# Performance work log

Hardware: AMD Instinct MI355X
Metric: run time of the kernel (lower is better)

Reference implementation:

```python
import jax, jax.numpy as jnp
import numpy as np

DIM = 1024
HEADS = 16
HEAD_DIM = 64
INNER = HEADS * HEAD_DIM  # 1024
SCALE = 8.0
LN_EPS = 1e-5
NORM_EPS = 1e-12  # F.normalize default eps


def layer_norm(x, g, b):
    m = jnp.mean(x, axis=-1, keepdims=True)
    v = jnp.mean((x - m) ** 2, axis=-1, keepdims=True)
    return (x - m) * jax.lax.rsqrt(v + LN_EPS) * g + b


def l2_normalize(x):
    n = jnp.sqrt(jnp.sum(x * x, axis=-1, keepdims=True))
    return x / jnp.maximum(n, NORM_EPS)


def setup_inputs() -> dict:
    key = jax.random.key(0)
    ks = jax.random.split(key, 8)
    B, N, T = 4, 4096, 256
    s = 0.02
    return {
        "x": jax.random.normal(ks[0], (B, N, DIM), jnp.float32),
        "context": jax.random.normal(ks[1], (B, T, DIM), jnp.float32),
        "Wq": jax.random.normal(ks[2], (DIM, INNER), jnp.float32) * s,
        "Wkv": jax.random.normal(ks[3], (DIM, 2 * INNER), jnp.float32) * s,
        "Wo": jax.random.normal(ks[4], (INNER, DIM), jnp.float32) * s,
        "null_kv": jax.random.normal(ks[5], (2, HEAD_DIM), jnp.float32),
        "q_scale": jnp.ones((HEAD_DIM,), jnp.float32),
        "k_scale": jnp.ones((HEAD_DIM,), jnp.float32),
        "ln_in_g": jnp.ones((DIM,), jnp.float32),
        "ln_in_b": jnp.zeros((DIM,), jnp.float32),
        "ln_ctx_g": jnp.ones((DIM,), jnp.float32),
        "ln_ctx_b": jnp.zeros((DIM,), jnp.float32),
        "ln_out_g": jnp.ones((DIM,), jnp.float32),
        "ln_out_b": jnp.zeros((DIM,), jnp.float32),
    }


def reference(x, context, Wq, Wkv, Wo, null_kv, q_scale, k_scale,
              ln_in_g, ln_in_b, ln_ctx_g, ln_ctx_b, ln_out_g, ln_out_b):
    B, N, _ = x.shape
    T = context.shape[1]
    xn = layer_norm(x, ln_in_g, ln_in_b)
    cn = layer_norm(context, ln_ctx_g, ln_ctx_b)
    q = xn @ Wq                      # [B, N, INNER]
    kv = cn @ Wkv                    # [B, T, 2*INNER]
    k, v = jnp.split(kv, 2, axis=-1)
    # split heads: b s (h d) -> b h s d
    def split_heads(t):
        b, s, _ = t.shape
        return t.reshape(b, s, HEADS, HEAD_DIM).transpose(0, 2, 1, 3)
    q, k, v = split_heads(q), split_heads(k), split_heads(v)
    # null kv token appended along kv-seq dim
    nk = jnp.broadcast_to(null_kv[0], (B, HEADS, 1, HEAD_DIM))
    nv = jnp.broadcast_to(null_kv[1], (B, HEADS, 1, HEAD_DIM))
    k = jnp.concatenate([k, nk], axis=2)   # [B, H, T+1, D]
    v = jnp.concatenate([v, nv], axis=2)
    q = l2_normalize(q) * q_scale
    k = l2_normalize(k) * k_scale
    scores = jnp.einsum('bhid,bhkd->bhik', q, k) * SCALE
    attn = jax.nn.softmax(scores, axis=-1)
    out = jnp.einsum('bhik,bhkd->bhid', attn, v)   # [B, H, N, D]
    out = out.transpose(0, 2, 1, 3).reshape(B, N, INNER)
    out = out @ Wo
    return layer_norm(out, ln_out_g, ln_out_b)
```

## Files before the change

### kernel.cpp

```cpp
#include <hip/hip_runtime.h>
#include <cstdint>
#include <cstddef>

typedef _Float16 f16;
typedef _Float16 f16x4 __attribute__((ext_vector_type(4)));
typedef _Float16 f16x8 __attribute__((ext_vector_type(8)));
typedef float f32x4 __attribute__((ext_vector_type(4)));
typedef __fp16 h16x2 __attribute__((ext_vector_type(2)));

#define DIM 1024
#define B_ 4
#define N_ 4096
#define TKP 288
#define SCALE_ 8.0f
#define LOG2E 1.4426950408889634f

__device__ __forceinline__ void gload_lds16(const void* g, void* l) {
  __builtin_amdgcn_global_load_lds(
      reinterpret_cast<const __attribute__((address_space(1))) uint32_t*>(
          reinterpret_cast<uintptr_t>(g)),
      reinterpret_cast<__attribute__((address_space(3))) uint32_t*>(
          reinterpret_cast<uintptr_t>(l)),
      16, 0, 0);
}

__global__ void transpose_w_kernel(const float* __restrict__ W, f16* __restrict__ WT,
                                   int K, int N) {
  __shared__ float tile[32][33];
  int nt = N >> 5;
  int tk = blockIdx.x / nt, tn = blockIdx.x % nt;
  int tx = threadIdx.x & 31, ty = threadIdx.x >> 5;
#pragma unroll
  for (int p = 0; p < 32; p += 8)
    tile[ty + p][tx] = W[(size_t)(tk * 32 + ty + p) * N + tn * 32 + tx];
  __syncthreads();
#pragma unroll
  for (int p = 0; p < 32; p += 8)
    WT[(size_t)(tn * 32 + ty + p) * K + tk * 32 + tx] = (f16)tile[tx][ty + p];
}

template <typename IN_T, typename OUT_T>
__global__ void ln_kernel(const IN_T* __restrict__ in, const float* __restrict__ g,
                          const float* __restrict__ bb, OUT_T* __restrict__ out) {
  int row = blockIdx.x;
  int t = threadIdx.x;
  float4 v;
  if constexpr (sizeof(IN_T) == 2) {
    f16x4 h = ((const f16x4*)((const f16*)in + (size_t)row * DIM))[t];
    v = {(float)h[0], (float)h[1], (float)h[2], (float)h[3]};
  } else {
    v = ((const float4*)((const float*)in + (size_t)row * DIM))[t];
  }
  float s = v.x + v.y + v.z + v.w;
  float ss = v.x * v.x + v.y * v.y + v.z * v.z + v.w * v.w;
#pragma unroll
  for (int m = 1; m < 64; m <<= 1) { s += __shfl_xor(s, m); ss += __shfl_xor(ss, m); }
  __shared__ float red[8];
  int w = t >> 6;
  if ((t & 63) == 0) { red[w * 2] = s; red[w * 2 + 1] = ss; }
  __syncthreads();
  s = red[0] + red[2] + red[4] + red[6];
  ss = red[1] + red[3] + red[5] + red[7];
  float mean = s * (1.0f / DIM);
  float var = ss * (1.0f / DIM) - mean * mean;
  float rstd = rsqrtf(var + 1e-5f);
  float4 gv = ((const float4*)g)[t];
  float4 bv = ((const float4*)bb)[t];
  float o0 = (v.x - mean) * rstd * gv.x + bv.x;
  float o1 = (v.y - mean) * rstd * gv.y + bv.y;
  float o2 = (v.z - mean) * rstd * gv.z + bv.z;
  float o3 = (v.w - mean) * rstd * gv.w + bv.w;
  if constexpr (sizeof(OUT_T) == 2) {
    f16x4 h = {(f16)o0, (f16)o1, (f16)o2, (f16)o3};
    *(f16x4*)((f16*)out + (size_t)row * DIM + t * 4) = h;
  } else {
    float4 o = {o0, o1, o2, o3};
    *(float4*)((float*)out + (size_t)row * DIM + t * 4) = o;
  }
}

template <bool OUT_F32>
__global__ __launch_bounds__(256, 2) void gemm_nt_kernel(
    const f16* __restrict__ A, const f16* __restrict__ Bt, void* __restrict__ C,
    int M, int N, int K) {
  __shared__ f16 As[128 * 64];
  __shared__ f16 Bs[128 * 64];
  int nb = N >> 7;
  int cpx = gridDim.x >> 3;
  int wg = ((int)blockIdx.x & 7) * cpx + ((int)blockIdx.x >> 3);
  int bm = wg / nb, bn = wg % nb;
  int t = threadIdx.x;
  int lane = t & 63, w = t >> 6;
  int wm = w >> 1, wn = w & 1;
  int r16 = lane & 15, g4 = lane >> 4;
  f32x4 acc[4][4] = {};
  for (int k0 = 0; k0 < K; k0 += 64) {
#pragma unroll
    for (int i = 0; i < 4; ++i) {
      int li = i * 256 + t;
      int r = li >> 3, c = li & 7;
      int kc = ((c ^ (r & 7)) << 3);
      gload_lds16(A + (size_t)(bm * 128 + r) * K + k0 + kc, (char*)As + li * 16);
      gload_lds16(Bt + (size_t)(bn * 128 + r) * K + k0 + kc, (char*)Bs + li * 16);
    }
    asm volatile("s_waitcnt vmcnt(0)" ::: "memory");
    __syncthreads();
#pragma unroll
    for (int ks = 0; ks < 2; ++ks) {
      f16x8 af[4], bf[4];
#pragma unroll
      for (int mi = 0; mi < 4; ++mi) {
        int r = wm * 64 + mi * 16 + r16;
        int cidx = ks * 4 + g4;
        af[mi] = *(const f16x8*)(As + r * 64 + ((cidx ^ (r & 7)) << 3));
      }
#pragma unroll
      for (int ni = 0; ni < 4; ++ni) {
        int r = wn * 64 + ni * 16 + r16;
        int cidx = ks * 4 + g4;
        bf[ni] = *(const f16x8*)(Bs + r * 64 + ((cidx ^ (r & 7)) << 3));
      }
#pragma unroll
      for (int mi = 0; mi < 4; ++mi)
#pragma unroll
        for (int ni = 0; ni < 4; ++ni)
          acc[mi][ni] = __builtin_amdgcn_mfma_f32_16x16x32_f16(af[mi], bf[ni],
                                                               acc[mi][ni], 0, 0, 0);
    }
    __syncthreads();
  }
  int cr0 = bm * 128 + wm * 64;
  int cc = bn * 128 + wn * 64 + r16;
#pragma unroll
  for (int mi = 0; mi < 4; ++mi)
#pragma unroll
    for (int ni = 0; ni < 4; ++ni)
#pragma unroll
      for (int j = 0; j < 4; ++j) {
        int row = cr0 + mi * 16 + g4 * 4 + j;
        int col = cc + ni * 16;
        if constexpr (OUT_F32)
          ((float*)C)[(size_t)row * N + col] = acc[mi][ni][j];
        else
          ((f16*)C)[(size_t)row * N + col] = (f16)acc[mi][ni][j];
      }
}

__global__ void prep_kv_kernel(const f16* __restrict__ kv, const float* __restrict__ nullkv,
                               const float* __restrict__ ks, f16* __restrict__ Karr,
                               f16* __restrict__ Varr) {
  int bh = blockIdx.x;
  int b = bh >> 4, h = bh & 15;
  int t = threadIdx.x;
  __shared__ f16 vt[256][65];
  const f16* krow = kv + (size_t)(b * 256 + t) * 2048 + h * 64;
  const f16* vrow = krow + 1024;
  f16x8 kd[8];
  float ss = 0.0f;
#pragma unroll
  for (int i = 0; i < 8; ++i) {
    kd[i] = *(const f16x8*)(krow + i * 8);
#pragma unroll
    for (int j = 0; j < 8; ++j) { float x = (float)kd[i][j]; ss += x * x; }
  }
  float inv = 1.0f / fmaxf(sqrtf(ss), 1e-12f);
  f16* kout = Karr + ((size_t)bh * TKP + t) * 64;
#pragma unroll
  for (int i = 0; i < 8; ++i) {
    f16x8 o;
#pragma unroll
    for (int j = 0; j < 8; ++j) o[j] = (f16)((float)kd[i][j] * inv * ks[i * 8 + j]);
    *(f16x8*)(kout + i * 8) = o;
  }
#pragma unroll
  for (int i = 0; i < 8; ++i) {
    f16x8 vv = *(const f16x8*)(vrow + i * 8);
#pragma unroll
    for (int j = 0; j < 8; ++j) vt[t][i * 8 + j] = vv[j];
  }
  if (t < 32) {
    f16* kr = Karr + ((size_t)bh * TKP + 256 + t) * 64;
    if (t == 0) {
      float ssn = 0.0f;
      for (int d = 0; d < 64; ++d) ssn += nullkv[d] * nullkv[d];
      float invn = 1.0f / fmaxf(sqrtf(ssn), 1e-12f);
      for (int d = 0; d < 64; ++d) kr[d] = (f16)(nullkv[d] * invn * ks[d]);
    } else {
      for (int d = 0; d < 64; ++d) kr[d] = (f16)0.0f;
    }
  }
  __syncthreads();
  f16* vbase = Varr + (size_t)bh * 64 * TKP;
  int pcol = (t & ~31) | (((t & 15) << 1) | ((t >> 4) & 1));
  for (int d = 0; d < 64; ++d) vbase[(size_t)d * TKP + pcol] = vt[t][d];
#pragma unroll
  for (int i = 0; i < 8; ++i) {
    int idx = i * 256 + t;
    int d = idx >> 5, key = 256 + (idx & 31);
    vbase[(size_t)d * TKP + key] = (key == 256) ? (f16)nullkv[64 + d] : (f16)0.0f;
  }
}

__global__ __launch_bounds__(256, 4) void attn_kernel(
    const f16* __restrict__ Q, const f16* __restrict__ Karr,
    const f16* __restrict__ Varr, const float* __restrict__ qs,
    const float* __restrict__ ksc, f16* __restrict__ O) {
  int wgid = ((int)blockIdx.x & 7) * 256 + ((int)blockIdx.x >> 3);
  int qb = wgid & 31, bh = wgid >> 5;
  int b = bh >> 4, h = bh & 15;
  int t = threadIdx.x, lane = t & 63, w = t >> 6;
  int r16 = lane & 15, g4 = lane >> 4;
  int row0 = b * N_ + qb * 128 + w * 32;
  int col0 = h * 64;
  const f16* Kp = Karr + (size_t)bh * TKP * 64;
  const f16* Vp = Varr + (size_t)bh * 64 * TKP;
  __shared__ f16 Plds[4][32 * 40];
  f16* Pw = &Plds[w][0];
  float mq = fabsf(qs[lane]), mk = fabsf(ksc[lane]);
#pragma unroll
  for (int m = 1; m < 64; m <<= 1) {
    mq = fmaxf(mq, __shfl_xor(mq, m));
    mk = fmaxf(mk, __shfl_xor(mk, m));
  }
  const float c1 = SCALE_ * LOG2E;
  const float c2 = SCALE_ * mq * mk * LOG2E;
  float qsv[2][8];
#pragma unroll
  for (int kdh = 0; kdh < 2; ++kdh)
#pragma unroll
    for (int i = 0; i < 8; ++i) qsv[kdh][i] = qs[kdh * 32 + g4 * 8 + i];
  f16x8 qf[2][2];
#pragma unroll
  for (int mi = 0; mi < 2; ++mi) {
    float f[2][8];
    float ssq = 0.0f;
#pragma unroll
    for (int kdh = 0; kdh < 2; ++kdh) {
      f16x8 v = *(const f16x8*)(Q + (size_t)(row0 + mi * 16 + r16) * DIM +
                                col0 + kdh * 32 + g4 * 8);
#pragma unroll
      for (int i = 0; i < 8; ++i) { f[kdh][i] = (float)v[i]; ssq += f[kdh][i] * f[kdh][i]; }
    }
    ssq += __shfl_xor(ssq, 16);
    ssq += __shfl_xor(ssq, 32);
    float inv = 1.0f / fmaxf(sqrtf(ssq), 1e-12f);
#pragma unroll
    for (int kdh = 0; kdh < 2; ++kdh) {
      f16x8 o;
#pragma unroll
      for (int i = 0; i < 8; ++i) o[i] = (f16)(f[kdh][i] * inv * qsv[kdh][i]);
      qf[mi][kdh] = o;
    }
  }
  f32x4 o[2][4] = {};
  float part[2][4] = {};
  const h16x2 ones2 = {(__fp16)1.0f, (__fp16)1.0f};
  f16x8 kf[2][2];
#pragma unroll
  for (int ni = 0; ni < 2; ++ni)
#pragma unroll
    for (int kdh = 0; kdh < 2; ++kdh)
      kf[ni][kdh] = *(const f16x8*)(Kp + (size_t)(ni * 16 + r16) * 64 +
                                    kdh * 32 + g4 * 8);
  for (int kt = 0; kt < 9; ++kt) {
    int key0 = kt * 32;
    f16x8 vf[4];
#pragma unroll
    for (int nd = 0; nd < 4; ++nd)
      vf[nd] = *(const f16x8*)(Vp + (size_t)(nd * 16 + r16) * TKP + key0 + g4 * 8);
    float nb0 = (key0 + r16 <= 256) ? -c2 : -(c2 + 128.0f);
    float nb1 = (key0 + 16 + r16 <= 256) ? -c2 : -(c2 + 128.0f);
    f32x4 s[2][2] = {};
    __builtin_amdgcn_s_setprio(1);
#pragma unroll
    for (int kdh = 0; kdh < 2; ++kdh)
#pragma unroll
      for (int mi = 0; mi < 2; ++mi)
#pragma unroll
        for (int ni = 0; ni < 2; ++ni)
          s[mi][ni] = __builtin_amdgcn_mfma_f32_16x16x32_f16(qf[mi][kdh], kf[ni][kdh],
                                                             s[mi][ni], 0, 0, 0);
    __builtin_amdgcn_s_setprio(0);
    if (kt < 8) {
#pragma unroll
      for (int ni = 0; ni < 2; ++ni)
#pragma unroll
        for (int kdh = 0; kdh < 2; ++kdh)
          kf[ni][kdh] = *(const f16x8*)(Kp + (size_t)(key0 + 32 + ni * 16 + r16) * 64 +
                                        kdh * 32 + g4 * 8);
    }
#pragma unroll
    for (int mi = 0; mi < 2; ++mi) {
#pragma unroll
      for (int j = 0; j < 4; ++j) {
        float p0 = __builtin_amdgcn_exp2f(s[mi][0][j] * c1 + nb0);
        float p1 = __builtin_amdgcn_exp2f(s[mi][1][j] * c1 + nb1);
        h16x2 pk = __builtin_amdgcn_cvt_pkrtz(p0, p1);
        part[mi][j] = __builtin_amdgcn_fdot2(pk, ones2, part[mi][j], false);
        int prow = mi * 16 + g4 * 4 + j;
        ((uint32_t*)(Pw + prow * 40))[r16] = __builtin_bit_cast(uint32_t, pk);
      }
    }
    __builtin_amdgcn_s_setprio(1);
#pragma unroll
    for (int mi = 0; mi < 2; ++mi) {
      f16x8 pa = *(const f16x8*)(Pw + (mi * 16 + r16) * 40 + g4 * 8);
#pragma unroll
      for (int nd = 0; nd < 4; ++nd)
        o[mi][nd] = __builtin_amdgcn_mfma_f32_16x16x32_f16(pa, vf[nd], o[mi][nd], 0, 0, 0);
    }
    __builtin_amdgcn_s_setprio(0);
  }
#pragma unroll
  for (int mi = 0; mi < 2; ++mi)
#pragma unroll
    for (int j = 0; j < 4; ++j) {
      float v = part[mi][j];
      v += __shfl_xor(v, 1); v += __shfl_xor(v, 2);
      v += __shfl_xor(v, 4); v += __shfl_xor(v, 8);
      part[mi][j] = v;
    }
#pragma unroll
  for (int mi = 0; mi < 2; ++mi)
#pragma unroll
    for (int j = 0; j < 4; ++j) {
      float inv = 1.0f / part[mi][j];
      int row = row0 + mi * 16 + g4 * 4 + j;
#pragma unroll
      for (int nd = 0; nd < 4; ++nd)
        O[(size_t)row * DIM + col0 + nd * 16 + r16] = (f16)(o[mi][nd][j] * inv);
    }
}

extern "C" void kernel_launch(void* const* d_in, const int* in_sizes, int n_in,
                              void* d_out, int out_size, void* d_ws, size_t ws_size,
                              hipStream_t stream) {
  const float* x      = (const float*)d_in[0];
  const float* ctx    = (const float*)d_in[1];
  const float* Wq     = (const float*)d_in[2];
  const float* Wkv    = (const float*)d_in[3];
  const float* Wo     = (const float*)d_in[4];
  const float* nullkv = (const float*)d_in[5];
  const float* qs     = (const float*)d_in[6];
  const float* ks     = (const float*)d_in[7];
  const float* g_in   = (const float*)d_in[8];
  const float* b_in   = (const float*)d_in[9];
  const float* g_ctx  = (const float*)d_in[10];
  const float* b_ctx  = (const float*)d_in[11];
  const float* g_out  = (const float*)d_in[12];
  const float* b_out  = (const float*)d_in[13];

  char* ws = (char*)d_ws;
  const size_t MB = 1ull << 20;
  f16* wqT   = (f16*)(ws + 0);
  f16* wkvT  = (f16*)(ws + 2 * MB);
  f16* woT   = (f16*)(ws + 6 * MB);
  f16* karr  = (f16*)(ws + 8 * MB);
  f16* varr  = (f16*)(ws + 11 * MB);
  f16* cn    = (f16*)(ws + 14 * MB);
  f16* kvb   = (f16*)(ws + 16 * MB);
  f16* xn    = (f16*)(ws + 20 * MB);
  f16* q_raw = (f16*)(ws + 52 * MB);
  f16* aout  = (f16*)(ws + 20 * MB);
  f16* out2h = (f16*)(ws + 52 * MB);

  transpose_w_kernel<<<1024, 256, 0, stream>>>(Wq, wqT, 1024, 1024);
  transpose_w_kernel<<<2048, 256, 0, stream>>>(Wkv, wkvT, 1024, 2048);
  transpose_w_kernel<<<1024, 256, 0, stream>>>(Wo, woT, 1024, 1024);

  ln_kernel<float, f16><<<16384, 256, 0, stream>>>(x, g_in, b_in, xn);
  ln_kernel<float, f16><<<1024, 256, 0, stream>>>(ctx, g_ctx, b_ctx, cn);

  gemm_nt_kernel<false><<<(16384 / 128) * (1024 / 128), 256, 0, stream>>>(
      xn, wqT, (void*)q_raw, 16384, 1024, 1024);
  gemm_nt_kernel<false><<<(1024 / 128) * (2048 / 128), 256, 0, stream>>>(
      cn, wkvT, (void*)kvb, 1024, 2048, 1024);

  prep_kv_kernel<<<64, 256, 0, stream>>>(kvb, nullkv, ks, karr, varr);

  attn_kernel<<<2048, 256, 0, stream>>>(q_raw, karr, varr, qs, ks, aout);

  gemm_nt_kernel<false><<<(16384 / 128) * (1024 / 128), 256, 0, stream>>>(
      aout, woT, (void*)out2h, 16384, 1024, 1024);

  ln_kernel<f16, float><<<16384, 256, 0, stream>>>(out2h, g_out, b_out, (float*)d_out);
}
```

Baseline: 339.5 us.

## Stage attention K/V through double-buffered LDS and merge small prep kernels

The attention kernel now copies each 32-key K and V tile into swizzled, double-buffered shared memory with async global-to-LDS loads. The next tile is prefetched while the current one is computed, with a block barrier each iteration. Before, every wave loaded its K and V fragments straight from global memory. Separately, the three weight transposes and the two input layer norms are each merged into one launch, and the explicit vmcnt wait before the GEMM barrier is dropped. The merges cut launch overhead. The new barriers and the reliance on barrier-implied waits for the LDS DMA add sync cost and some correctness risk.

```diff
diff --git a/kernel.cpp b/kernel.cpp
--- a/kernel.cpp
+++ b/kernel.cpp
@@ -24,11 +24,19 @@
       16, 0, 0);
 }
 
-__global__ void transpose_w_kernel(const float* __restrict__ W, f16* __restrict__ WT,
-                                   int K, int N) {
+__global__ void transpose_all_kernel(const float* __restrict__ Wq,
+                                     const float* __restrict__ Wkv,
+                                     const float* __restrict__ Wo,
+                                     f16* __restrict__ wqT, f16* __restrict__ wkvT,
+                                     f16* __restrict__ woT) {
+  int bid = blockIdx.x;
+  const float* W; f16* WT; int K = 1024, N; int tb;
+  if (bid < 1024)      { W = Wq;  WT = wqT;  N = 1024; tb = bid; }
+  else if (bid < 3072) { W = Wkv; WT = wkvT; N = 2048; tb = bid - 1024; }
+  else                 { W = Wo;  WT = woT;  N = 1024; tb = bid - 3072; }
   __shared__ float tile[32][33];
   int nt = N >> 5;
-  int tk = blockIdx.x / nt, tn = blockIdx.x % nt;
+  int tk = tb / nt, tn = tb % nt;
   int tx = threadIdx.x & 31, ty = threadIdx.x >> 5;
 #pragma unroll
   for (int p = 0; p < 32; p += 8)
@@ -39,18 +47,8 @@
     WT[(size_t)(tn * 32 + ty + p) * K + tk * 32 + tx] = (f16)tile[tx][ty + p];
 }
 
-template <typename IN_T, typename OUT_T>
-__global__ void ln_kernel(const IN_T* __restrict__ in, const float* __restrict__ g,
-                          const float* __restrict__ bb, OUT_T* __restrict__ out) {
-  int row = blockIdx.x;
-  int t = threadIdx.x;
-  float4 v;
-  if constexpr (sizeof(IN_T) == 2) {
-    f16x4 h = ((const f16x4*)((const f16*)in + (size_t)row * DIM))[t];
-    v = {(float)h[0], (float)h[1], (float)h[2], (float)h[3]};
-  } else {
-    v = ((const float4*)((const float*)in + (size_t)row * DIM))[t];
-  }
+__device__ __forceinline__ void ln_row_f16out(const float4 v, const float* g,
+                                              const float* bb, int t, f16* outrow) {
   float s = v.x + v.y + v.z + v.w;
   float ss = v.x * v.x + v.y * v.y + v.z * v.z + v.w * v.w;
 #pragma unroll
@@ -66,17 +64,50 @@
   float rstd = rsqrtf(var + 1e-5f);
   float4 gv = ((const float4*)g)[t];
   float4 bv = ((const float4*)bb)[t];
-  float o0 = (v.x - mean) * rstd * gv.x + bv.x;
-  float o1 = (v.y - mean) * rstd * gv.y + bv.y;
-  float o2 = (v.z - mean) * rstd * gv.z + bv.z;
-  float o3 = (v.w - mean) * rstd * gv.w + bv.w;
-  if constexpr (sizeof(OUT_T) == 2) {
-    f16x4 h = {(f16)o0, (f16)o1, (f16)o2, (f16)o3};
-    *(f16x4*)((f16*)out + (size_t)row * DIM + t * 4) = h;
-  } else {
-    float4 o = {o0, o1, o2, o3};
-    *(float4*)((float*)out + (size_t)row * DIM + t * 4) = o;
-  }
+  f16x4 h = {(f16)((v.x - mean) * rstd * gv.x + bv.x),
+             (f16)((v.y - mean) * rstd * gv.y + bv.y),
+             (f16)((v.z - mean) * rstd * gv.z + bv.z),
+             (f16)((v.w - mean) * rstd * gv.w + bv.w)};
+  *(f16x4*)(outrow + t * 4) = h;
+}
+
+__global__ void ln_xc_kernel(const float* __restrict__ x, const float* __restrict__ ctx,
+                             const float* __restrict__ gx, const float* __restrict__ bx,
+                             const float* __restrict__ gc, const float* __restrict__ bc,
+                             f16* __restrict__ xn, f16* __restrict__ cn) {
+  int row = blockIdx.x;
+  int t = threadIdx.x;
+  const float* in; const float* g; const float* bb; f16* out; int r;
+  if (row < 16384) { in = x; g = gx; bb = bx; out = xn; r = row; }
+  else             { in = ctx; g = gc; bb = bc; out = cn; r = row - 16384; }
+  float4 v = ((const float4*)(in + (size_t)r * DIM))[t];
+  ln_row_f16out(v, g, bb, t, out + (size_t)r * DIM);
+}
+
+__global__ void ln_out_kernel(const f16* __restrict__ in, const float* __restrict__ g,
+                              const float* __restrict__ bb, float* __restrict__ out) {
+  int row = blockIdx.x;
+  int t = threadIdx.x;
+  f16x4 h = ((const f16x4*)(in + (size_t)row * DIM))[t];
+  float4 v = {(float)h[0], (float)h[1], (float)h[2], (float)h[3]};
+  float s = v.x + v.y + v.z + v.w;
+  float ss = v.x * v.x + v.y * v.y + v.z * v.z + v.w * v.w;
+#pragma unroll
+  for (int m = 1; m < 64; m <<= 1) { s += __shfl_xor(s, m); ss += __shfl_xor(ss, m); }
+  __shared__ float red[8];
+  int w = t >> 6;
+  if ((t & 63) == 0) { red[w * 2] = s; red[w * 2 + 1] = ss; }
+  __syncthreads();
+  s = red[0] + red[2] + red[4] + red[6];
+  ss = red[1] + red[3] + red[5] + red[7];
+  float mean = s * (1.0f / DIM);
+  float var = ss * (1.0f / DIM) - mean * mean;
+  float rstd = rsqrtf(var + 1e-5f);
+  float4 gv = ((const float4*)g)[t];
+  float4 bv = ((const float4*)bb)[t];
+  float4 o = {(v.x - mean) * rstd * gv.x + bv.x, (v.y - mean) * rstd * gv.y + bv.y,
+              (v.z - mean) * rstd * gv.z + bv.z, (v.w - mean) * rstd * gv.w + bv.w};
+  *(float4*)(out + (size_t)row * DIM + t * 4) = o;
 }
 
 template <bool OUT_F32>
@@ -103,7 +134,6 @@
       gload_lds16(A + (size_t)(bm * 128 + r) * K + k0 + kc, (char*)As + li * 16);
       gload_lds16(Bt + (size_t)(bn * 128 + r) * K + k0 + kc, (char*)Bs + li * 16);
     }
-    asm volatile("s_waitcnt vmcnt(0)" ::: "memory");
     __syncthreads();
 #pragma unroll
     for (int ks = 0; ks < 2; ++ks) {
@@ -214,8 +244,14 @@
   int col0 = h * 64;
   const f16* Kp = Karr + (size_t)bh * TKP * 64;
   const f16* Vp = Varr + (size_t)bh * 64 * TKP;
+  __shared__ f16 Ks[2][32 * 64];
+  __shared__ f16 Vs[2][64 * 32];
   __shared__ f16 Plds[4][32 * 40];
   f16* Pw = &Plds[w][0];
+  int krow_s = t >> 3;
+  int kc_s = (t & 7) ^ (krow_s & 7);
+  int vrow_s = t >> 2;
+  int vc_s = (t & 3) ^ ((vrow_s >> 1) & 3);
   float mq = fabsf(qs[lane]), mk = fabsf(ksc[lane]);
 #pragma unroll
   for (int m = 1; m < 64; m <<= 1) {
@@ -224,6 +260,8 @@
   }
   const float c1 = SCALE_ * LOG2E;
   const float c2 = SCALE_ * mq * mk * LOG2E;
+  gload_lds16(Kp + (size_t)krow_s * 64 + kc_s * 8, (char*)Ks[0] + t * 16);
+  gload_lds16(Vp + (size_t)vrow_s * TKP + 0 + vc_s * 8, (char*)Vs[0] + t * 16);
   float qsv[2][8];
 #pragma unroll
   for (int kdh = 0; kdh < 2; ++kdh)
@@ -255,21 +293,27 @@
   f32x4 o[2][4] = {};
   float part[2][4] = {};
   const h16x2 ones2 = {(__fp16)1.0f, (__fp16)1.0f};
-  f16x8 kf[2][2];
-#pragma unroll
-  for (int ni = 0; ni < 2; ++ni)
-#pragma unroll
-    for (int kdh = 0; kdh < 2; ++kdh)
-      kf[ni][kdh] = *(const f16x8*)(Kp + (size_t)(ni * 16 + r16) * 64 +
-                                    kdh * 32 + g4 * 8);
+  __syncthreads();
+#pragma unroll
   for (int kt = 0; kt < 9; ++kt) {
-    int key0 = kt * 32;
-    f16x8 vf[4];
-#pragma unroll
-    for (int nd = 0; nd < 4; ++nd)
-      vf[nd] = *(const f16x8*)(Vp + (size_t)(nd * 16 + r16) * TKP + key0 + g4 * 8);
-    float nb0 = (key0 + r16 <= 256) ? -c2 : -(c2 + 128.0f);
-    float nb1 = (key0 + 16 + r16 <= 256) ? -c2 : -(c2 + 128.0f);
+    const int cur = kt & 1;
+    const int key0 = kt * 32;
+    if (kt < 8) {
+      const int nxt = key0 + 32;
+      gload_lds16(Kp + (size_t)(nxt + krow_s) * 64 + kc_s * 8,
+                  (char*)Ks[cur ^ 1] + t * 16);
+      gload_lds16(Vp + (size_t)vrow_s * TKP + nxt + vc_s * 8,
+                  (char*)Vs[cur ^ 1] + t * 16);
+    }
+    f16x8 kf[2][2];
+#pragma unroll
+    for (int ni = 0; ni < 2; ++ni)
+#pragma unroll
+      for (int kdh = 0; kdh < 2; ++kdh) {
+        int row = ni * 16 + r16;
+        int cidx = kdh * 4 + g4;
+        kf[ni][kdh] = *(const f16x8*)(Ks[cur] + row * 64 + ((cidx ^ (row & 7)) << 3));
+      }
     f32x4 s[2][2] = {};
     __builtin_amdgcn_s_setprio(1);
 #pragma unroll
@@ -281,14 +325,8 @@
           s[mi][ni] = __builtin_amdgcn_mfma_f32_16x16x32_f16(qf[mi][kdh], kf[ni][kdh],
                                                              s[mi][ni], 0, 0, 0);
     __builtin_amdgcn_s_setprio(0);
-    if (kt < 8) {
-#pragma unroll
-      for (int ni = 0; ni < 2; ++ni)
-#pragma unroll
-        for (int kdh = 0; kdh < 2; ++kdh)
-          kf[ni][kdh] = *(const f16x8*)(Kp + (size_t)(key0 + 32 + ni * 16 + r16) * 64 +
-                                        kdh * 32 + g4 * 8);
-    }
+    float nb0 = (key0 + r16 <= 256) ? -c2 : -(c2 + 128.0f);
+    float nb1 = (key0 + 16 + r16 <= 256) ? -c2 : -(c2 + 128.0f);
 #pragma unroll
     for (int mi = 0; mi < 2; ++mi) {
 #pragma unroll
@@ -301,6 +339,13 @@
         ((uint32_t*)(Pw + prow * 40))[r16] = __builtin_bit_cast(uint32_t, pk);
       }
     }
+    f16x8 vf[4];
+#pragma unroll
+    for (int nd = 0; nd < 4; ++nd) {
+      int row = nd * 16 + r16;
+      int slot = g4 ^ ((row >> 1) & 3);
+      vf[nd] = *(const f16x8*)(Vs[cur] + row * 32 + (slot << 3));
+    }
     __builtin_amdgcn_s_setprio(1);
 #pragma unroll
     for (int mi = 0; mi < 2; ++mi) {
@@ -310,6 +355,7 @@
         o[mi][nd] = __builtin_amdgcn_mfma_f32_16x16x32_f16(pa, vf[nd], o[mi][nd], 0, 0, 0);
     }
     __builtin_amdgcn_s_setprio(0);
+    __syncthreads();
   }
 #pragma unroll
   for (int mi = 0; mi < 2; ++mi)
@@ -364,12 +410,10 @@
   f16* aout  = (f16*)(ws + 20 * MB);
   f16* out2h = (f16*)(ws + 52 * MB);
 
-  transpose_w_kernel<<<1024, 256, 0, stream>>>(Wq, wqT, 1024, 1024);
-  transpose_w_kernel<<<2048, 256, 0, stream>>>(Wkv, wkvT, 1024, 2048);
-  transpose_w_kernel<<<1024, 256, 0, stream>>>(Wo, woT, 1024, 1024);
-
-  ln_kernel<float, f16><<<16384, 256, 0, stream>>>(x, g_in, b_in, xn);
-  ln_kernel<float, f16><<<1024, 256, 0, stream>>>(ctx, g_ctx, b_ctx, cn);
+  transpose_all_kernel<<<4096, 256, 0, stream>>>(Wq, Wkv, Wo, wqT, wkvT, woT);
+
+  ln_xc_kernel<<<16384 + 1024, 256, 0, stream>>>(x, ctx, g_in, b_in, g_ctx, b_ctx,
+                                                 xn, cn);
 
   gemm_nt_kernel<false><<<(16384 / 128) * (1024 / 128), 256, 0, stream>>>(
       xn, wqT, (void*)q_raw, 16384, 1024, 1024);
@@ -383,5 +427,5 @@
   gemm_nt_kernel<false><<<(16384 / 128) * (1024 / 128), 256, 0, stream>>>(
       aout, woT, (void*)out2h, 16384, 1024, 1024);
 
-  ln_kernel<f16, float><<<16384, 256, 0, stream>>>(out2h, g_out, b_out, (float*)d_out);
-}
+  ln_out_kernel<<<16384, 256, 0, stream>>>(out2h, g_out, b_out, (float*)d_out);
+}
```

Result: faster. 330.2 us (-2.8%).
